# Performance work log

Hardware: AMD Instinct MI355X
Metric: run time of the kernel (lower is better)

The kernel has to match this reference:

```python
import jax, jax.numpy as jnp
import numpy as np

N, K, C_IN, C_OUT = 30000, 16, 128, 256


def setup_inputs() -> dict:
    key = jax.random.key(0)
    ks = jax.random.split(key, 8)
    s1 = 1.0 / np.sqrt(2 * C_IN)
    s2 = 1.0 / np.sqrt(C_OUT)
    s3 = 1.0 / np.sqrt(C_IN)
    return {
        "feat": jax.random.normal(ks[0], (N, C_IN), dtype=jnp.float32),
        "knn_idx": jax.random.randint(ks[1], (N, K), 0, N, dtype=jnp.int64),
        "W1": jax.random.uniform(ks[2], (2 * C_IN, C_OUT), jnp.float32, -s1, s1),
        "b1": jax.random.uniform(ks[3], (C_OUT,), jnp.float32, -s1, s1),
        "W2": jax.random.uniform(ks[4], (C_OUT, C_OUT), jnp.float32, -s2, s2),
        "b2": jax.random.uniform(ks[5], (C_OUT,), jnp.float32, -s2, s2),
        "Ws": jax.random.uniform(ks[6], (C_IN, C_OUT), jnp.float32, -s3, s3),
        "bs": jax.random.uniform(ks[7], (C_OUT,), jnp.float32, -s3, s3),
        "gamma": jnp.ones((C_OUT,), jnp.float32),
        "beta": jnp.zeros((C_OUT,), jnp.float32),
    }


def _layer_norm(x, gamma, beta, eps=1e-5):
    mu = jnp.mean(x, axis=-1, keepdims=True)
    var = jnp.var(x, axis=-1, keepdims=True)
    return (x - mu) * jax.lax.rsqrt(var + eps) * gamma + beta


def reference(feat, knn_idx, W1, b1, W2, b2, Ws, bs, gamma, beta):
    # gather neighbors: (N, K, C_in)
    neighbor = feat[knn_idx]
    center = feat[:, None, :]  # broadcast over K
    # edge feature: concat(center, neighbor - center) -> (N, K, 2*C_in)
    edge = jnp.concatenate([jnp.broadcast_to(center, neighbor.shape), neighbor - center], axis=-1)
    # edge MLP: Linear -> exact GELU -> Linear
    h = jax.nn.gelu(jnp.einsum("nkc,cd->nkd", edge, W1) + b1, approximate=False)
    edge_out = jnp.einsum("nkd,de->nke", h, W2) + b2  # (N, K, C_out)
    agg = jnp.max(edge_out, axis=1)  # (N, C_out)
    skip = feat @ Ws + bs
    return _layer_norm(agg + skip, gamma, beta)
```

## Files before the change

kernel.cpp:

```cpp
#include <hip/hip_runtime.h>
#include <hip/hip_bf16.h>
#include <math.h>

#define NPTS 30000
#define KNN  16
#define NB   30
#define GRID 250

typedef __attribute__((ext_vector_type(8)))  __bf16 bf16x8;
typedef __attribute__((ext_vector_type(16))) float  f32x16;
typedef __attribute__((ext_vector_type(4)))  float  f32x4;

__device__ __forceinline__ unsigned short f2bf(float x) {
    __bf16 b = (__bf16)x;
    return __builtin_bit_cast(unsigned short, b);
}
__device__ __forceinline__ unsigned pk2(float a, float b) {
    return (unsigned)f2bf(a) | ((unsigned)f2bf(b) << 16);
}
__device__ __forceinline__ float bf_lo(unsigned u) { return __builtin_bit_cast(float, u << 16); }
__device__ __forceinline__ float bf_hi(unsigned u) { return __builtin_bit_cast(float, u & 0xffff0000u); }
__device__ __forceinline__ float gelu_t(float x) {
    float x2 = x * x;
    float u  = x * fmaf(0.07135481624f, x2, 1.59576912161f);
    float e  = __expf(u);
    float r  = __builtin_amdgcn_rcpf(e + 1.0f);
    return fmaf(-x, r, x);
}

__global__ void prep_w(const float* __restrict__ W1, const float* __restrict__ W2,
                       const float* __restrict__ Ws,
                       unsigned short* __restrict__ w1dt, unsigned short* __restrict__ w2t,
                       unsigned short* __restrict__ wcst) {
    int t = blockIdx.x * 256 + threadIdx.x;
    {   int e = t >> 8, c = t & 255;
        w2t[t] = f2bf(W2[c * 256 + e]); }
    {   int col = t >> 7, k = t & 127;
        float v = (col < 256) ? W1[k * 256 + col] : Ws[k * 256 + (col - 256)];
        wcst[t] = f2bf(v); }
    if (t < 32768) {
        int d = t >> 7, k = t & 127;
        w1dt[t] = f2bf(W1[(128 + k) * 256 + d]); }
}

__global__ __launch_bounds__(512, 1) void edgeconv_main(
    const float* __restrict__ feat, const int* __restrict__ knn,
    const unsigned short* __restrict__ w1dt, const unsigned short* __restrict__ w2t,
    const unsigned short* __restrict__ wcst,
    const float* __restrict__ b1, const float* __restrict__ b2,
    const float* __restrict__ bs,
    const float* __restrict__ gamma, const float* __restrict__ beta,
    float* __restrict__ out)
{
    __shared__ __align__(16) unsigned char  s_edge[2][64 * 256];
    __shared__ __align__(16) unsigned char  s_h[2][64 * 512];
    __shared__ __align__(16) unsigned short s_c2[2][16][512];
    __shared__ __align__(16) float s_agg[2][4][256];

    const int lane = threadIdx.x & 63;
    const int wv   = threadIdx.x >> 6;
    const int l31  = lane & 31;
    const int lh   = lane >> 5;
    const int l15  = lane & 15;
    const int l4   = lane >> 4;
    const int pblock = blockIdx.x * 120;
    const int chb = wv * 32;

    bf16x8 w1f[8], w2f[16];
    #pragma unroll
    for (int ks = 0; ks < 8; ++ks)
        w1f[ks] = *(const bf16x8*)(w1dt + (chb + l31) * 128 + ks * 16 + lh * 8);
    #pragma unroll
    for (int ks = 0; ks < 16; ++ks)
        w2f[ks] = *(const bf16x8*)(w2t + (chb + l31) * 256 + ks * 16 + lh * 8);

    auto c2pass = [&](int s) {
        const int buf = s & 1;
        const int pb  = pblock + s * 16;
        bf16x8 af[4];
        #pragma unroll
        for (int ks = 0; ks < 4; ++ks) {
            int p = pb + l15; p = (p < NPTS) ? p : (NPTS - 1);
            const float* fp = feat + (long)p * 128 + ks * 32 + l4 * 8;
            float4 f0 = *(const float4*)fp;
            float4 f1 = *(const float4*)(fp + 4);
            uint4 u;
            u.x = pk2(f0.x, f0.y); u.y = pk2(f0.z, f0.w);
            u.z = pk2(f1.x, f1.y); u.w = pk2(f1.z, f1.w);
            af[ks] = __builtin_bit_cast(bf16x8, u);
        }
        #pragma unroll
        for (int j = 0; j < 4; ++j) {
            const int ct  = wv * 4 + j;
            const int col = ct * 16 + l15;
            float bias = (ct < 16) ? b1[col] : (bs[col - 256] + b2[col - 256]);
            f32x4 acc = {bias, bias, bias, bias};
            #pragma unroll
            for (int ks = 0; ks < 4; ++ks) {
                bf16x8 bf = *(const bf16x8*)(wcst + col * 128 + ks * 32 + l4 * 8);
                acc = __builtin_amdgcn_mfma_f32_16x16x32_bf16(af[ks], bf, acc, 0, 0, 0);
            }
            #pragma unroll
            for (int r = 0; r < 4; ++r)
                s_c2[buf][l4 * 4 + r][col] = f2bf(acc[r]);
        }
    };

    const int st_pt = wv >> 1;
    const int st_kb = (wv & 1) * 8;

    {
        const int n = pblock + st_pt;
        float2 cc = *(const float2*)(feat + (long)n * 128 + lane * 2);
        #pragma unroll
        for (int kk = 0; kk < 8; ++kk) {
            int idx = knn[n * 16 + st_kb + kk];
            float2 nb = *(const float2*)(feat + (long)idx * 128 + lane * 2);
            int row = st_pt * 16 + st_kb + kk;
            unsigned v = pk2(nb.x - cc.x, nb.y - cc.y);
            *(unsigned*)(s_edge[0] + row * 256 + ((unsigned)(lane * 4) ^ (unsigned)((row & 15) << 4))) = v;
        }
    }
    c2pass(0);
    __syncthreads();

    const f32x16 z16 = (f32x16)0.0f;

    #pragma unroll 1
    for (int i = 0; i <= NB + 1; ++i) {
        float2 cc; float2 nbr[8];
        const bool doStage = (i + 1 < NB);
        if (doStage) {
            const int n = pblock + (i + 1) * 4 + st_pt;
            cc = *(const float2*)(feat + (long)n * 128 + lane * 2);
            int idx[8];
            #pragma unroll
            for (int kk = 0; kk < 8; ++kk) idx[kk] = knn[n * 16 + st_kb + kk];
            #pragma unroll
            for (int kk = 0; kk < 8; ++kk)
                nbr[kk] = *(const float2*)(feat + (long)idx[kk] * 128 + lane * 2);
        }

        if (i >= 1 && i <= NB) {
            const int bt = i - 1;
            #pragma unroll
            for (int rowb = 0; rowb < 2; ++rowb) {
                const int row = rowb * 32 + l31;
                const unsigned swz = (unsigned)((row & 31) << 4);
                const unsigned rb = (unsigned)row * 512u;
                f32x16 a2 = z16;
                #pragma unroll
                for (int ks = 0; ks < 16; ++ks) {
                    bf16x8 hf = *(const bf16x8*)(s_h[bt & 1] + rb + ((unsigned)(ks * 32 + lh * 16) ^ swz));
                    a2 = __builtin_amdgcn_mfma_f32_32x32x16_bf16(hf, w2f[ks], a2, 0, 0, 0);
                }
                float m0 = a2[0], m1 = a2[8];
                #pragma unroll
                for (int r = 1; r < 8; ++r) {
                    m0 = fmaxf(m0, a2[r]);
                    m1 = fmaxf(m1, a2[8 + r]);
                }
                m0 = fmaxf(m0, __shfl_xor(m0, 32));
                m1 = fmaxf(m1, __shfl_xor(m1, 32));
                if (lh == 0) {
                    s_agg[bt & 1][rowb * 2 + 0][chb + l31] = m0;
                    s_agg[bt & 1][rowb * 2 + 1][chb + l31] = m1;
                }
            }
        }

        if (i < NB) {
            const int sB = (i >> 2) & 1;
            f32x16 acc1[2] = {z16, z16};
            #pragma unroll
            for (int rowb = 0; rowb < 2; ++rowb) {
                const int row = rowb * 32 + l31;
                const unsigned swz = (unsigned)((row & 15) << 4);
                const unsigned rb = (unsigned)row * 256u;
                #pragma unroll
                for (int ks = 0; ks < 8; ++ks) {
                    bf16x8 bf = *(const bf16x8*)(s_edge[i & 1] + rb + ((unsigned)(ks * 32 + lh * 16) ^ swz));
                    acc1[rowb] = __builtin_amdgcn_mfma_f32_32x32x16_bf16(w1f[ks], bf, acc1[rowb], 0, 0, 0);
                }
            }
            #pragma unroll
            for (int rowb = 0; rowb < 2; ++rowb) {
                const int row  = rowb * 32 + l31;
                const int pt16 = (i & 3) * 4 + rowb * 2 + (l31 >> 4);
                const unsigned swz = (unsigned)((row & 31) << 4);
                #pragma unroll
                for (int g = 0; g < 4; ++g) {
                    const int ch0 = chb + 8 * g + 4 * lh;
                    uint2 c2v = *(const uint2*)(&s_c2[sB][pt16][ch0]);
                    float v0 = gelu_t(acc1[rowb][4 * g + 0] + bf_lo(c2v.x));
                    float v1 = gelu_t(acc1[rowb][4 * g + 1] + bf_hi(c2v.x));
                    float v2 = gelu_t(acc1[rowb][4 * g + 2] + bf_lo(c2v.y));
                    float v3 = gelu_t(acc1[rowb][4 * g + 3] + bf_hi(c2v.y));
                    uint2 hv; hv.x = pk2(v0, v1); hv.y = pk2(v2, v3);
                    *(uint2*)(s_h[i & 1] + (unsigned)row * 512u + ((unsigned)(ch0 * 2) ^ swz)) = hv;
                }
            }
        }

        if (i >= 2 && wv < 4) {
            const int bt2 = i - 2;
            const int n   = pblock + bt2 * 4 + wv;
            const int sB  = (bt2 >> 2) & 1;
            const int pt16 = (bt2 & 3) * 4 + wv;
            float4 ag = *(const float4*)&s_agg[bt2 & 1][wv][lane * 4];
            uint2 sk  = *(const uint2*)(&s_c2[sB][pt16][256 + lane * 4]);
            float x0 = ag.x + bf_lo(sk.x), x1 = ag.y + bf_hi(sk.x);
            float x2 = ag.z + bf_lo(sk.y), x3 = ag.w + bf_hi(sk.y);
            float s  = x0 + x1 + x2 + x3;
            float ss = fmaf(x0, x0, fmaf(x1, x1, fmaf(x2, x2, x3 * x3)));
            #pragma unroll
            for (int off = 1; off < 64; off <<= 1) {
                s  += __shfl_xor(s, off);
                ss += __shfl_xor(ss, off);
            }
            float mu   = s * (1.0f / 256.0f);
            float var  = ss * (1.0f / 256.0f) - mu * mu;
            float rstd = rsqrtf(var + 1e-5f);
            float4 g4 = *(const float4*)&gamma[lane * 4];
            float4 b4 = *(const float4*)&beta[lane * 4];
            float4 o;
            o.x = (x0 - mu) * rstd * g4.x + b4.x;
            o.y = (x1 - mu) * rstd * g4.y + b4.y;
            o.z = (x2 - mu) * rstd * g4.z + b4.z;
            o.w = (x3 - mu) * rstd * g4.w + b4.w;
            *(float4*)&out[(long)n * 256 + lane * 4] = o;
        }

        if ((i & 3) == 2) {
            int s = (i + 2) >> 2;
            if (s < 8) c2pass(s);
        }

        if (doStage) {
            const int bt = i + 1;
            #pragma unroll
            for (int kk = 0; kk < 8; ++kk) {
                int row = st_pt * 16 + st_kb + kk;
                unsigned v = pk2(nbr[kk].x - cc.x, nbr[kk].y - cc.y);
                *(unsigned*)(s_edge[bt & 1] + row * 256 + ((unsigned)(lane * 4) ^ (unsigned)((row & 15) << 4))) = v;
            }
        }
        __syncthreads();
    }
}

extern "C" void kernel_launch(void* const* d_in, const int* in_sizes, int n_in,
                              void* d_out, int out_size, void* d_ws, size_t ws_size,
                              hipStream_t stream) {
    const float* feat  = (const float*)d_in[0];
    const int*   knn   = (const int*)  d_in[1];
    const float* W1    = (const float*)d_in[2];
    const float* b1    = (const float*)d_in[3];
    const float* W2    = (const float*)d_in[4];
    const float* b2    = (const float*)d_in[5];
    const float* Ws    = (const float*)d_in[6];
    const float* bs    = (const float*)d_in[7];
    const float* gamma = (const float*)d_in[8];
    const float* beta  = (const float*)d_in[9];
    float* out = (float*)d_out;

    unsigned short* w1dt = (unsigned short*)d_ws;
    unsigned short* w2t  = w1dt + 32768;
    unsigned short* wcst = w2t + 65536;

    hipLaunchKernelGGL(prep_w, dim3(256), dim3(256), 0, stream, W1, W2, Ws, w1dt, w2t, wcst);
    hipLaunchKernelGGL(edgeconv_main, dim3(GRID), dim3(512), 0, stream,
                       feat, knn, w1dt, w2t, wcst, b1, b2, bs, gamma, beta, out);
}
```

Baseline: 201.9 us.

## Halve per-block point tile to run two blocks per CU on 500 blocks

```diff
diff --git a/kernel.cpp b/kernel.cpp
--- a/kernel.cpp
+++ b/kernel.cpp
@@ -5,7 +5,7 @@
 #define NPTS 30000
 #define KNN  16
 #define NB   30
-#define GRID 250
+#define GRID 500
 
 typedef __attribute__((ext_vector_type(8)))  __bf16 bf16x8;
 typedef __attribute__((ext_vector_type(16))) float  f32x16;
@@ -43,7 +43,7 @@
         w1dt[t] = f2bf(W1[(128 + k) * 256 + d]); }
 }
 
-__global__ __launch_bounds__(512, 1) void edgeconv_main(
+__global__ __launch_bounds__(512) void edgeconv_main(
     const float* __restrict__ feat, const int* __restrict__ knn,
     const unsigned short* __restrict__ w1dt, const unsigned short* __restrict__ w2t,
     const unsigned short* __restrict__ wcst,
@@ -52,10 +52,10 @@
     const float* __restrict__ gamma, const float* __restrict__ beta,
     float* __restrict__ out)
 {
-    __shared__ __align__(16) unsigned char  s_edge[2][64 * 256];
-    __shared__ __align__(16) unsigned char  s_h[2][64 * 512];
-    __shared__ __align__(16) unsigned short s_c2[2][16][512];
-    __shared__ __align__(16) float s_agg[2][4][256];
+    __shared__ __align__(16) unsigned char  s_edge[2][32 * 256];
+    __shared__ __align__(16) unsigned char  s_h[2][32 * 512];
+    __shared__ __align__(16) unsigned short s_c2[2][8][512];
+    __shared__ __align__(16) float s_agg[2][2][256];
 
     const int lane = threadIdx.x & 63;
     const int wv   = threadIdx.x >> 6;
@@ -63,7 +63,7 @@
     const int lh   = lane >> 5;
     const int l15  = lane & 15;
     const int l4   = lane >> 4;
-    const int pblock = blockIdx.x * 120;
+    const int pblock = blockIdx.x * 60;
     const int chb = wv * 32;
 
     bf16x8 w1f[8], w2f[16];
@@ -76,12 +76,12 @@
 
     auto c2pass = [&](int s) {
         const int buf = s & 1;
-        const int pb  = pblock + s * 16;
         bf16x8 af[4];
         #pragma unroll
         for (int ks = 0; ks < 4; ++ks) {
-            int p = pb + l15; p = (p < NPTS) ? p : (NPTS - 1);
-            const float* fp = feat + (long)p * 128 + ks * 32 + l4 * 8;
+            int pi = s * 8 + (l15 & 7);
+            if (pi > 59) pi = 59;
+            const float* fp = feat + (long)(pblock + pi) * 128 + ks * 32 + l4 * 8;
             float4 f0 = *(const float4*)fp;
             float4 f1 = *(const float4*)(fp + 4);
             uint4 u;
@@ -101,26 +101,31 @@
                 acc = __builtin_amdgcn_mfma_f32_16x16x32_bf16(af[ks], bf, acc, 0, 0, 0);
             }
             #pragma unroll
-            for (int r = 0; r < 4; ++r)
-                s_c2[buf][l4 * 4 + r][col] = f2bf(acc[r]);
+            for (int r = 0; r < 4; ++r) {
+                int prow = l4 * 4 + r;
+                if (prow < 8) s_c2[buf][prow][col] = f2bf(acc[r]);
+            }
         }
     };
 
-    const int st_pt = wv >> 1;
-    const int st_kb = (wv & 1) * 8;
-
-    {
-        const int n = pblock + st_pt;
+    auto stage = [&](int bt) {
+        const int st_pt = wv >> 2;
+        const int st_kb = (wv & 3) * 4;
+        const int n = pblock + bt * 2 + st_pt;
         float2 cc = *(const float2*)(feat + (long)n * 128 + lane * 2);
-        #pragma unroll
-        for (int kk = 0; kk < 8; ++kk) {
-            int idx = knn[n * 16 + st_kb + kk];
-            float2 nb = *(const float2*)(feat + (long)idx * 128 + lane * 2);
+        int idx[4];
+        #pragma unroll
+        for (int kk = 0; kk < 4; ++kk) idx[kk] = knn[n * 16 + st_kb + kk];
+        #pragma unroll
+        for (int kk = 0; kk < 4; ++kk) {
+            float2 nb = *(const float2*)(feat + (long)idx[kk] * 128 + lane * 2);
             int row = st_pt * 16 + st_kb + kk;
             unsigned v = pk2(nb.x - cc.x, nb.y - cc.y);
-            *(unsigned*)(s_edge[0] + row * 256 + ((unsigned)(lane * 4) ^ (unsigned)((row & 15) << 4))) = v;
-        }
-    }
+            *(unsigned*)(s_edge[bt & 1] + row * 256 + ((unsigned)(lane * 4) ^ (unsigned)((row & 15) << 4))) = v;
+        }
+    };
+
+    stage(0);
     c2pass(0);
     __syncthreads();
 
@@ -128,87 +133,68 @@
 
     #pragma unroll 1
     for (int i = 0; i <= NB + 1; ++i) {
-        float2 cc; float2 nbr[8];
-        const bool doStage = (i + 1 < NB);
-        if (doStage) {
-            const int n = pblock + (i + 1) * 4 + st_pt;
-            cc = *(const float2*)(feat + (long)n * 128 + lane * 2);
-            int idx[8];
-            #pragma unroll
-            for (int kk = 0; kk < 8; ++kk) idx[kk] = knn[n * 16 + st_kb + kk];
-            #pragma unroll
-            for (int kk = 0; kk < 8; ++kk)
-                nbr[kk] = *(const float2*)(feat + (long)idx[kk] * 128 + lane * 2);
-        }
-
         if (i >= 1 && i <= NB) {
             const int bt = i - 1;
-            #pragma unroll
-            for (int rowb = 0; rowb < 2; ++rowb) {
-                const int row = rowb * 32 + l31;
-                const unsigned swz = (unsigned)((row & 31) << 4);
-                const unsigned rb = (unsigned)row * 512u;
-                f32x16 a2 = z16;
-                #pragma unroll
-                for (int ks = 0; ks < 16; ++ks) {
-                    bf16x8 hf = *(const bf16x8*)(s_h[bt & 1] + rb + ((unsigned)(ks * 32 + lh * 16) ^ swz));
-                    a2 = __builtin_amdgcn_mfma_f32_32x32x16_bf16(hf, w2f[ks], a2, 0, 0, 0);
-                }
-                float m0 = a2[0], m1 = a2[8];
-                #pragma unroll
-                for (int r = 1; r < 8; ++r) {
-                    m0 = fmaxf(m0, a2[r]);
-                    m1 = fmaxf(m1, a2[8 + r]);
-                }
-                m0 = fmaxf(m0, __shfl_xor(m0, 32));
-                m1 = fmaxf(m1, __shfl_xor(m1, 32));
-                if (lh == 0) {
-                    s_agg[bt & 1][rowb * 2 + 0][chb + l31] = m0;
-                    s_agg[bt & 1][rowb * 2 + 1][chb + l31] = m1;
-                }
+            const int row = l31;
+            const unsigned swz = (unsigned)((row & 31) << 4);
+            const unsigned rb = (unsigned)row * 512u;
+            f32x16 a2 = z16;
+            #pragma unroll
+            for (int ks = 0; ks < 16; ++ks) {
+                bf16x8 hf = *(const bf16x8*)(s_h[bt & 1] + rb + ((unsigned)(ks * 32 + lh * 16) ^ swz));
+                a2 = __builtin_amdgcn_mfma_f32_32x32x16_bf16(hf, w2f[ks], a2, 0, 0, 0);
+            }
+            float m0 = a2[0], m1 = a2[8];
+            #pragma unroll
+            for (int r = 1; r < 8; ++r) {
+                m0 = fmaxf(m0, a2[r]);
+                m1 = fmaxf(m1, a2[8 + r]);
+            }
+            m0 = fmaxf(m0, __shfl_xor(m0, 32));
+            m1 = fmaxf(m1, __shfl_xor(m1, 32));
+            if (lh == 0) {
+                s_agg[bt & 1][0][chb + l31] = m0;
+                s_agg[bt & 1][1][chb + l31] = m1;
             }
         }
 
         if (i < NB) {
             const int sB = (i >> 2) & 1;
-            f32x16 acc1[2] = {z16, z16};
-            #pragma unroll
-            for (int rowb = 0; rowb < 2; ++rowb) {
-                const int row = rowb * 32 + l31;
+            const int row = l31;
+            f32x16 acc1 = z16;
+            {
                 const unsigned swz = (unsigned)((row & 15) << 4);
                 const unsigned rb = (unsigned)row * 256u;
                 #pragma unroll
                 for (int ks = 0; ks < 8; ++ks) {
                     bf16x8 bf = *(const bf16x8*)(s_edge[i & 1] + rb + ((unsigned)(ks * 32 + lh * 16) ^ swz));
-                    acc1[rowb] = __builtin_amdgcn_mfma_f32_32x32x16_bf16(w1f[ks], bf, acc1[rowb], 0, 0, 0);
+                    acc1 = __builtin_amdgcn_mfma_f32_32x32x16_bf16(w1f[ks], bf, acc1, 0, 0, 0);
                 }
             }
-            #pragma unroll
-            for (int rowb = 0; rowb < 2; ++rowb) {
-                const int row  = rowb * 32 + l31;
-                const int pt16 = (i & 3) * 4 + rowb * 2 + (l31 >> 4);
+            {
+                const int pt8 = (i & 3) * 2 + (l31 >> 4);
                 const unsigned swz = (unsigned)((row & 31) << 4);
                 #pragma unroll
                 for (int g = 0; g < 4; ++g) {
                     const int ch0 = chb + 8 * g + 4 * lh;
-                    uint2 c2v = *(const uint2*)(&s_c2[sB][pt16][ch0]);
-                    float v0 = gelu_t(acc1[rowb][4 * g + 0] + bf_lo(c2v.x));
-                    float v1 = gelu_t(acc1[rowb][4 * g + 1] + bf_hi(c2v.x));
-                    float v2 = gelu_t(acc1[rowb][4 * g + 2] + bf_lo(c2v.y));
-                    float v3 = gelu_t(acc1[rowb][4 * g + 3] + bf_hi(c2v.y));
+                    uint2 c2v = *(const uint2*)(&s_c2[sB][pt8][ch0]);
+                    float v0 = gelu_t(acc1[4 * g + 0] + bf_lo(c2v.x));
+                    float v1 = gelu_t(acc1[4 * g + 1] + bf_hi(c2v.x));
+                    float v2 = gelu_t(acc1[4 * g + 2] + bf_lo(c2v.y));
+                    float v3 = gelu_t(acc1[4 * g + 3] + bf_hi(c2v.y));
                     uint2 hv; hv.x = pk2(v0, v1); hv.y = pk2(v2, v3);
                     *(uint2*)(s_h[i & 1] + (unsigned)row * 512u + ((unsigned)(ch0 * 2) ^ swz)) = hv;
                 }
             }
         }
 
-        if (i >= 2 && wv < 4) {
+        if (i >= 2 && wv < 2) {
             const int bt2 = i - 2;
-            const int n   = pblock + bt2 * 4 + wv;
+            const int n   = pblock + bt2 * 2 + wv;
             const int sB  = (bt2 >> 2) & 1;
-            const int pt16 = (bt2 & 3) * 4 + wv;
+            const int pt8 = (bt2 & 3) * 2 + wv;
             float4 ag = *(const float4*)&s_agg[bt2 & 1][wv][lane * 4];
-            uint2 sk  = *(const uint2*)(&s_c2[sB][pt16][256 + lane * 4]);
+            uint2 sk  = *(const uint2*)(&s_c2[sB][pt8][256 + lane * 4]);
             float x0 = ag.x + bf_lo(sk.x), x1 = ag.y + bf_hi(sk.x);
             float x2 = ag.z + bf_lo(sk.y), x3 = ag.w + bf_hi(sk.y);
             float s  = x0 + x1 + x2 + x3;
@@ -232,19 +218,12 @@
         }
 
         if ((i & 3) == 2) {
-            int s = (i + 2) >> 2;
+            int s = (i >> 2) + 1;
             if (s < 8) c2pass(s);
         }
 
-        if (doStage) {
-            const int bt = i + 1;
-            #pragma unroll
-            for (int kk = 0; kk < 8; ++kk) {
-                int row = st_pt * 16 + st_kb + kk;
-                unsigned v = pk2(nbr[kk].x - cc.x, nbr[kk].y - cc.y);
-                *(unsigned*)(s_edge[bt & 1] + row * 256 + ((unsigned)(lane * 4) ^ (unsigned)((row & 15) << 4))) = v;
-            }
-        }
+        if (i + 1 < NB) stage(i + 1);
+
         __syncthreads();
     }
 }
```

Result: slower. 256.5 us (+27.1%).
